# Kernel optimization log

Hardware: AMD Instinct MI355X
Metric: run time of the kernel (lower is better)

Reference implementation:

```python
import jax, jax.numpy as jnp
import numpy as np

T, D, NPER, K = 8192, 512, 4, 6  # minority samples, dims, synthetic-per-sample, SMOTE k


def setup_inputs() -> dict:
    key = jax.random.key(0)
    k1, k2, k3 = jax.random.split(key, 3)
    min_samples = jax.random.normal(k1, (T, D), dtype=jnp.float32)
    gaps = jax.random.uniform(k2, (T, NPER), dtype=jnp.float32)
    # populate() draws randint(0, k-2) inclusive -> values in [0, K-1) = [0, 5)
    nn_choice = jax.random.randint(k3, (T, NPER), 0, K - 1, dtype=jnp.int64)
    return {"min_samples": min_samples, "gaps": gaps, "nn_choice": nn_choice}


def reference(min_samples, gaps, nn_choice):
    # --- find_k: full pairwise euclidean distance matrix [T, T] ---
    sq = jnp.sum(min_samples * min_samples, axis=1)  # [T]
    d2 = sq[:, None] + sq[None, :] - 2.0 * (min_samples @ min_samples.T)
    dist = jnp.sqrt(jnp.maximum(d2, 0.0))  # [T, T]
    # --- k_neighbors: argsort rows, drop self (col 0), keep k-1 neighbors ---
    nn_idx = jnp.argsort(dist, axis=1)[:, 1:K]  # [T, K-1] int
    # --- populate: pick a random neighbor, interpolate with random gap ---
    neigh = jnp.take_along_axis(nn_idx, nn_choice, axis=1)  # [T, NPER]
    diff = min_samples[neigh] - min_samples[:, None, :]      # [T, NPER, D]
    syn = min_samples[:, None, :] + gaps[:, :, None] * diff  # [T, NPER, D]
    # row-major reshape matches the original's (outer i, inner N) fill order
    return syn.reshape(T * NPER, D)
```

## Files before the change

### kernel.cpp

```cpp
#include <hip/hip_runtime.h>
#include <cstdint>
#include <cstddef>

#define TN   8192
#define DD   512
#define NPER 4
#define KNN  5

typedef _Float16 f16x8 __attribute__((ext_vector_type(8)));
typedef float    f32x4 __attribute__((ext_vector_type(4)));
typedef unsigned int  u32;
typedef unsigned long long u64;

#define KSCALE (-1.1920928955078125e-07f)

__device__ __forceinline__ u32 pk32(float key, int idx) {
  u32 kb = __float_as_uint(key) ^ 0x80000000u;
  return (kb & 0xFFFFE000u) | (u32)idx;
}

__device__ __forceinline__ void swins5(u32 v, u32 t[5]) {
#pragma unroll
  for (int s = 0; s < 5; ++s) {
    u32 lo = v < t[s] ? v : t[s];
    u32 hi = v < t[s] ? t[s] : v;
    t[s] = lo; v = hi;
  }
}
__device__ __forceinline__ void swins8(u32 v, u32 t[8]) {
#pragma unroll
  for (int s = 0; s < 8; ++s) {
    u32 lo = v < t[s] ? v : t[s];
    u32 hi = v < t[s] ? t[s] : v;
    t[s] = lo; v = hi;
  }
}

__device__ __forceinline__ u64 packkey64(float key, int idx) {
  u32 kb = __float_as_uint(key);
  kb ^= (((int)kb >> 31) | 0x80000000u);
  return ((u64)kb << 32) | (u32)idx;
}
__device__ __forceinline__ void ins8_64(u64 v, u64 tv[8]) {
  if (v < tv[7]) {
    tv[7] = v;
#pragma unroll
    for (int s = 7; s > 0; --s) {
      u64 lo = tv[s] < tv[s-1] ? tv[s] : tv[s-1];
      u64 hi = tv[s] < tv[s-1] ? tv[s-1] : tv[s];
      tv[s-1] = lo; tv[s] = hi;
    }
  }
}

__global__ void prep_blk(const float* __restrict__ X, _Float16* __restrict__ Hb,
                         float* __restrict__ rowsq) {
  __shared__ float rs[16];
  const int rb16 = (int)blockIdx.x;
  const int tid  = (int)threadIdx.x;
  const int lane = tid & 63;
  const int wv   = tid >> 6;
  const int lgrp = lane >> 4;
  const int lidx = lane & 15;
  if (tid < 16) rs[tid] = 0.f;
  __syncthreads();
  const float* src = X + (size_t)(rb16*16 + lidx) * DD + lgrp*8;
  float psum = 0.f;
#pragma unroll
  for (int i = 0; i < 4; ++i) {
    const int kc = wv*4 + i;
    const float4 x0 = *(const float4*)(src + kc*32);
    const float4 x1 = *(const float4*)(src + kc*32 + 4);
    float xs[8] = {x0.x, x0.y, x0.z, x0.w, x1.x, x1.y, x1.z, x1.w};
    f16x8 h;
#pragma unroll
    for (int j = 0; j < 8; ++j) {
      h[j] = (_Float16)(xs[j] * 4096.f);
      psum = fmaf(xs[j], xs[j], psum);
    }
    *(f16x8*)((char*)Hb + ((size_t)rb16*16 + kc)*1024 + lane*16) = h;
  }
  atomicAdd(&rs[lidx], psum);
  __syncthreads();
  if (tid < 16) rowsq[rb16*16 + tid] = rs[tid];
}

__launch_bounds__(256, 1)
__global__ void gemm_top8(const _Float16* __restrict__ Hb,
                          const float* __restrict__ rowsq, u32* __restrict__ partials) {
  __shared__ u32 mg[128 * 8];
  const int tid  = (int)threadIdx.x;
  const int lane = tid & 63;
  const int w    = tid >> 6;
  const int wr   = w >> 1, wc = w & 1;
  const int q    = ((int)blockIdx.x & 7) * 128 + ((int)blockIdx.x >> 3);
  const int cb   = q & 63;
  const int rsb  = q >> 6;
  const int jb   = cb * 128;
  const int lgrp = lane >> 4;
  const int lidx = lane & 15;

  const char* Bpb = (const char*)Hb + (size_t)(cb*8 + wc*4)*16384 + lane*16;

#define LOADF(dep, apb, ksv) do {                                               \
    _Pragma("unroll")                                                           \
    for (int t = 0; t < 4; ++t)                                                 \
      fa[dep][t] = *(const f16x8*)((apb) + t*16384 + (ksv)*1024);               \
    _Pragma("unroll")                                                           \
    for (int u = 0; u < 4; ++u)                                                 \
      fb[dep][u] = *(const f16x8*)(Bpb + u*16384 + (ksv)*1024);                 \
  } while (0)

#define MFMAS(dep) do {                                                         \
    _Pragma("unroll")                                                           \
    for (int rt = 0; rt < 4; ++rt)                                              \
      _Pragma("unroll")                                                         \
      for (int cf = 0; cf < 4; ++cf)                                            \
        acc[rt][cf] = __builtin_amdgcn_mfma_f32_16x16x32_f16(fa[dep][rt],       \
                                        fb[dep][cf], acc[rt][cf], 0, 0, 0);     \
  } while (0)

  u32 t5[4][5];
#pragma unroll
  for (int c = 0; c < 4; ++c)
#pragma unroll
    for (int s = 0; s < 5; ++s) t5[c][s] = 0xFFFFFFFFu;

  for (int tt = 0; tt < 4; ++tt) {
    const int row0 = rsb * 512 + tt * 128;
    const char* Apb = (const char*)Hb + (size_t)(rsb*32 + tt*8 + wr*4)*16384 + lane*16;

    f32x4 acc[4][4] = {};
    f16x8 fa[3][4], fb[3][4];
    LOADF(0, Apb, 0);
    LOADF(1, Apb, 1);
    LOADF(2, Apb, 2);
#pragma unroll
    for (int ks = 0; ks < 16; ++ks) {
      const int d = ks % 3;
      MFMAS(d);
      if (ks + 3 < 16) LOADF(d, Apb, ks + 3);
    }

    float4 sqr[4];
#pragma unroll
    for (int t = 0; t < 4; ++t)
      sqr[t] = *(const float4*)(rowsq + row0 + wr*64 + t*16 + lgrp*4);

#pragma unroll
    for (int cf = 0; cf < 4; ++cf) {
      const int jc = jb + wc*64 + cf*16 + lidx;
#pragma unroll
      for (int t = 0; t < 4; ++t) {
        const int rbase = row0 + wr*64 + t*16 + lgrp*4;
        const float sx[4] = {sqr[t].x, sqr[t].y, sqr[t].z, sqr[t].w};
#pragma unroll
        for (int qq = 0; qq < 4; ++qq) {
          const int r = rbase + qq;
          const float key = fmaf(acc[t][cf][qq], KSCALE, sx[qq]);
          u32 v = pk32(key, r);
          v = (r == jc) ? 0xFFFFFFFFu : v;
          swins5(v, t5[cf]);
        }
      }
    }
  }

#pragma unroll
  for (int cf = 0; cf < 4; ++cf) {
    const int jc = jb + wc*64 + cf*16 + lidx;
    u32 t8[8];
#pragma unroll
    for (int s = 0; s < 5; ++s) t8[s] = t5[cf][s];
#pragma unroll
    for (int s = 5; s < 8; ++s) t8[s] = 0xFFFFFFFFu;
    {
      u32 ov[5];
#pragma unroll
      for (int s = 0; s < 5; ++s) ov[s] = __shfl_xor(t5[cf][s], 16, 64);
#pragma unroll
      for (int s = 0; s < 5; ++s) swins8(ov[s], t8);
    }
    {
      u32 ov[8];
#pragma unroll
      for (int s = 0; s < 8; ++s) ov[s] = __shfl_xor(t8[s], 32, 64);
#pragma unroll
      for (int s = 0; s < 8; ++s) swins8(ov[s], t8);
    }
    if (wr == 1 && lane < 16) {
#pragma unroll
      for (int s = 0; s < 8; ++s) mg[(wc*64 + cf*16 + lidx)*8 + s] = t8[s];
    }
    __syncthreads();
    if (wr == 0 && lane < 16) {
      const u32* om = &mg[(wc*64 + cf*16 + lidx)*8];
#pragma unroll
      for (int s = 0; s < 8; ++s) swins8(om[s], t8);
      u32* pw = partials + ((size_t)jc * 16 + rsb) * 8;
#pragma unroll
      for (int s = 0; s < 8; ++s) pw[s] = t8[s];
    }
    __syncthreads();
  }
#undef LOADF
#undef MFMAS
}

__global__ void merge_nn8(const u32* __restrict__ parts, u32* __restrict__ cand) {
  const int j    = (int)blockIdx.x * 4 + ((int)threadIdx.x >> 6);
  const int lane = (int)threadIdx.x & 63;
  u32 tv[8];
#pragma unroll
  for (int s = 0; s < 8; ++s) tv[s] = 0xFFFFFFFFu;
  swins8(parts[(size_t)j * 128 + lane], tv);
  swins8(parts[(size_t)j * 128 + 64 + lane], tv);
#pragma unroll
  for (int d = 1; d < 64; d <<= 1) {
    u32 ov[8];
#pragma unroll
    for (int s = 0; s < 8; ++s) ov[s] = __shfl_xor(tv[s], d, 64);
#pragma unroll
    for (int s = 0; s < 8; ++s) swins8(ov[s], tv);
  }
  if (lane == 0) {
#pragma unroll
    for (int s = 0; s < 8; ++s) cand[(size_t)j*8 + s] = tv[s];
  }
}

__global__ void refine_nn(const float* __restrict__ X, const float* __restrict__ rowsq,
                          const u32* __restrict__ cand, int* __restrict__ nn) {
  const int j    = (int)blockIdx.x * 4 + ((int)threadIdx.x >> 6);
  const int lane = (int)threadIdx.x & 63;
  const float4* xj = (const float4*)(X + (size_t)j * DD);
  const float4 qa = xj[lane];
  const float4 qb = xj[lane + 64];
  u64 best[8];
#pragma unroll
  for (int s = 0; s < 8; ++s) best[s] = ~0ull;
#pragma unroll
  for (int c = 0; c < 8; ++c) {
    const int r = (int)(cand[(size_t)j*8 + c] & 8191u);
    const float4* xr_ = (const float4*)(X + (size_t)r * DD);
    const float4 a = xr_[lane];
    const float4 b = xr_[lane + 64];
    float d = a.x*qa.x + a.y*qa.y + a.z*qa.z + a.w*qa.w
            + b.x*qb.x + b.y*qb.y + b.z*qb.z + b.w*qb.w;
#pragma unroll
    for (int off = 32; off >= 1; off >>= 1) d += __shfl_xor(d, off, 64);
    const float key = fmaf(-2.f, d, rowsq[r]);
    ins8_64(packkey64(key, r), best);
  }
  if (lane == 0) {
#pragma unroll
    for (int s = 0; s < KNN; ++s) nn[j*KNN + s] = (int)(u32)best[s];
  }
}

__global__ void synth_kernel(const float* __restrict__ X, const int* __restrict__ nn,
                             const float* __restrict__ gaps, const int* __restrict__ choice,
                             float* __restrict__ out) {
  const float4* X4 = (const float4*)X;
  float4* O4 = (float4*)out;
  const int base = (int)blockIdx.x * 256 + (int)threadIdx.x;
#pragma unroll
  for (int it = 0; it < 8; ++it) {
    const int f    = base + it * (2048 * 256);
    const int orow = f >> 7;
    const int d4   = f & 127;
    const int i    = orow >> 2;
    const int ch   = choice[orow];
    const int nr   = nn[i * KNN + ch];
    const float g  = gaps[orow];
    const float4 xi = X4[(size_t)i  * 128 + d4];
    const float4 xn = X4[(size_t)nr * 128 + d4];
    float4 r;
    r.x = fmaf(g, xn.x - xi.x, xi.x);
    r.y = fmaf(g, xn.y - xi.y, xi.y);
    r.z = fmaf(g, xn.z - xi.z, xi.z);
    r.w = fmaf(g, xn.w - xi.w, xi.w);
    O4[(size_t)orow * 128 + d4] = r;
  }
}

extern "C" void kernel_launch(void* const* d_in, const int* in_sizes, int n_in,
                              void* d_out, int out_size, void* d_ws, size_t ws_size,
                              hipStream_t stream) {
  const float* X      = (const float*)d_in[0];
  const float* gaps   = (const float*)d_in[1];
  const int*   choice = (const int*)  d_in[2];
  float* out = (float*)d_out;

  _Float16* Hb    = (_Float16*)d_out;
  u32*      parts = (u32*)((char*)d_out + 8388608);
  u32*      cand  = (u32*)((char*)d_out + 12582912);

  float* rowsq = (float*)d_ws;
  int*   nn    = (int*)((char*)d_ws + TN * 4);

  prep_blk    <<<512,  256, 0, stream>>>(X, Hb, rowsq);
  gemm_top8   <<<1024, 256, 0, stream>>>(Hb, rowsq, parts);
  merge_nn8   <<<2048, 256, 0, stream>>>(parts, cand);
  refine_nn   <<<2048, 256, 0, stream>>>(X, rowsq, cand, nn);
  synth_kernel<<<2048, 256, 0, stream>>>(X, nn, gaps, choice, out);
}
```

Before: 154.6 us.

## Stage B column panel in LDS via global_load_lds and deepen A prefetch

The gemm_top8 kernel now copies each block's 128-column B panel (128 KB of f16) into dynamic LDS once, using global_load_lds, and reads B fragments from LDS instead of global memory for every row tile. The A-operand register prefetch ring grows from 3 to 6 stages, and B uses a 2-stage ring from LDS. This is meant to cut redundant global and L2 traffic for B across the four row tiles and to hide A load latency better. In exchange the kernel uses about 132 KB of LDS per block, which limits occupancy to one block per CU, and it adds register pressure from the deeper A ring.

Result: slower. 295.1 us (+90.9%).

```diff
diff --git a/kernel.cpp b/kernel.cpp
--- a/kernel.cpp
+++ b/kernel.cpp
@@ -51,6 +51,12 @@
       tv[s-1] = lo; tv[s] = hi;
     }
   }
+}
+
+__device__ __forceinline__ void gll16(const void* g, void* l) {
+  __builtin_amdgcn_global_load_lds(
+      (const __attribute__((address_space(1))) void*)g,
+      (__attribute__((address_space(3))) void*)l, 16, 0, 0);
 }
 
 __global__ void prep_blk(const float* __restrict__ X, _Float16* __restrict__ Hb,
@@ -88,7 +94,8 @@
 __launch_bounds__(256, 1)
 __global__ void gemm_top8(const _Float16* __restrict__ Hb,
                           const float* __restrict__ rowsq, u32* __restrict__ partials) {
-  __shared__ u32 mg[128 * 8];
+  extern __shared__ __align__(16) char smem[];
+  u32* mg = (u32*)(smem + 131072);
   const int tid  = (int)threadIdx.x;
   const int lane = tid & 63;
   const int w    = tid >> 6;
@@ -100,24 +107,34 @@
   const int lgrp = lane >> 4;
   const int lidx = lane & 15;
 
-  const char* Bpb = (const char*)Hb + (size_t)(cb*8 + wc*4)*16384 + lane*16;
-
-#define LOADF(dep, apb, ksv) do {                                               \
+  {
+    const char* bsrc = (const char*)Hb + (size_t)(cb*8 + 2*w)*16384 + (size_t)lane*16;
+    char* bdst = smem + 2*w*16384;
+#pragma unroll
+    for (int c = 0; c < 32; ++c)
+      gll16(bsrc + c*1024, bdst + c*1024);
+  }
+  __syncthreads();
+
+#define LOADA(dep, ksv) do {                                                    \
     _Pragma("unroll")                                                           \
     for (int t = 0; t < 4; ++t)                                                 \
-      fa[dep][t] = *(const f16x8*)((apb) + t*16384 + (ksv)*1024);               \
+      fa[dep][t] = *(const f16x8*)(Apb + t*16384 + (ksv)*1024);                 \
+  } while (0)
+
+#define LOADB(dep, ksv) do {                                                    \
     _Pragma("unroll")                                                           \
     for (int u = 0; u < 4; ++u)                                                 \
-      fb[dep][u] = *(const f16x8*)(Bpb + u*16384 + (ksv)*1024);                 \
+      fb[dep][u] = *(const f16x8*)(smem + (wc*4+u)*16384 + (ksv)*1024 + lane*16); \
   } while (0)
 
-#define MFMAS(dep) do {                                                         \
+#define MFMAS(d6, d2) do {                                                      \
     _Pragma("unroll")                                                           \
     for (int rt = 0; rt < 4; ++rt)                                              \
       _Pragma("unroll")                                                         \
       for (int cf = 0; cf < 4; ++cf)                                            \
-        acc[rt][cf] = __builtin_amdgcn_mfma_f32_16x16x32_f16(fa[dep][rt],       \
-                                        fb[dep][cf], acc[rt][cf], 0, 0, 0);     \
+        acc[rt][cf] = __builtin_amdgcn_mfma_f32_16x16x32_f16(fa[d6][rt],        \
+                                        fb[d2][cf], acc[rt][cf], 0, 0, 0);      \
   } while (0)
 
   u32 t5[4][5];
@@ -131,15 +148,18 @@
     const char* Apb = (const char*)Hb + (size_t)(rsb*32 + tt*8 + wr*4)*16384 + lane*16;
 
     f32x4 acc[4][4] = {};
-    f16x8 fa[3][4], fb[3][4];
-    LOADF(0, Apb, 0);
-    LOADF(1, Apb, 1);
-    LOADF(2, Apb, 2);
+    f16x8 fa[6][4];
+    f16x8 fb[2][4];
+    LOADA(0, 0); LOADA(1, 1); LOADA(2, 2);
+    LOADA(3, 3); LOADA(4, 4); LOADA(5, 5);
+    LOADB(0, 0); LOADB(1, 1);
 #pragma unroll
     for (int ks = 0; ks < 16; ++ks) {
-      const int d = ks % 3;
-      MFMAS(d);
-      if (ks + 3 < 16) LOADF(d, Apb, ks + 3);
+      const int d6 = ks % 6;
+      const int d2 = ks & 1;
+      MFMAS(d6, d2);
+      if (ks + 6 < 16) LOADA(d6, ks + 6);
+      if (ks + 2 < 16) LOADB(d2, ks + 2);
     }
 
     float4 sqr[4];
@@ -203,7 +223,8 @@
     }
     __syncthreads();
   }
-#undef LOADF
+#undef LOADA
+#undef LOADB
 #undef MFMAS
 }
 
@@ -299,8 +320,11 @@
   float* rowsq = (float*)d_ws;
   int*   nn    = (int*)((char*)d_ws + TN * 4);
 
+  static_cast<void>(hipFuncSetAttribute((const void*)gemm_top8,
+      hipFuncAttributeMaxDynamicSharedMemorySize, 135168));
+
   prep_blk    <<<512,  256, 0, stream>>>(X, Hb, rowsq);
-  gemm_top8   <<<1024, 256, 0, stream>>>(Hb, rowsq, parts);
+  gemm_top8   <<<1024, 256, 135168, stream>>>(Hb, rowsq, parts);
   merge_nn8   <<<2048, 256, 0, stream>>>(parts, cand);
   refine_nn   <<<2048, 256, 0, stream>>>(X, rowsq, cand, nn);
   synth_kernel<<<2048, 256, 0, stream>>>(X, nn, gaps, choice, out);
```
